# Kernel tuning notes

Measured on AMD Instinct MI355X. Metric: run time of the kernel, lower is better.

The kernel has to match this reference:

```python
import jax, jax.numpy as jnp
import numpy as np

B, T, TA = 16, 512, 1024
D_REG, D_AUD, HID, HEADS = 512, 512, 256, 4
NREG = 4  # mouth, left_eye, right_eye, nose (dict order)
N = NREG * B * T + B * TA  # total graph nodes


def _build_edges():
    # Faithful, vectorized version of build_graph's edge construction (phoneme_times=None).
    bs = np.arange(B)[:, None]
    ts = np.arange(T)[None, :]
    src, dst = [], []
    # cross-region same-timestep edges, all ordered pairs i != j (edge_attr 0)
    for i in range(NREG):
        for j in range(NREG):
            if i != j:
                n1 = i * B * T + bs * T + ts
                n2 = j * B * T + bs * T + ts
                src.append(n1.ravel()); dst.append(n2.ravel())
    # temporal edges within each region (edge_attr 1)
    tt = np.arange(T - 1)[None, :]
    for i in range(NREG):
        n1 = i * B * T + bs * T + tt
        src.append(n1.ravel()); dst.append((n1 + 1).ravel())
    # eye (region idx 1,2) -> audio alignment edges (edge_attr 3)
    t_aud = (np.arange(T)[None, :] * TA) // T
    audio_start = NREG * B * T
    for i in (1, 2):
        n_eye = i * B * T + bs * T + ts
        n_aud = audio_start + bs * TA + t_aud
        src.append(n_eye.ravel()); dst.append(np.broadcast_to(n_aud, (B, T)).ravel())
    # self loops (PyG GATConv default add_self_loops=True)
    loops = np.arange(N)
    src.append(loops); dst.append(loops)
    return np.concatenate(src).astype(np.int32), np.concatenate(dst).astype(np.int32)


def setup_inputs() -> dict:
    key = jax.random.key(0)
    ks = iter(jax.random.split(key, 48))
    def rn(shape, scale=1.0):
        return jax.random.normal(next(ks), shape, dtype=jnp.float32) * jnp.float32(scale)
    src_np, dst_np = _build_edges()
    inp = {
        'mouth': rn((B, T, D_REG)), 'left_eye': rn((B, T, D_REG)),
        'right_eye': rn((B, T, D_REG)), 'nose': rn((B, T, D_REG)),
        'audio_embeddings': rn((B, TA, D_AUD)),
    }
    s = 1.0 / np.sqrt(D_REG)
    for name in ['mouth', 'left_eye', 'right_eye', 'nose']:
        inp['w_' + name] = rn((D_REG, HID), s)
        inp['b_' + name] = jnp.zeros((HID,), jnp.float32)
    inp['w_audio'] = rn((D_AUD, HID), 1.0 / np.sqrt(D_AUD))
    inp['b_audio'] = jnp.zeros((HID,), jnp.float32)
    # GAT layers: layer 0 in=HID, layers 1,2 in=HID*HEADS; layers 0,1 concat, layer 2 averages heads
    dims_in = [HID, HID * HEADS, HID * HEADS]
    for l, din in enumerate(dims_in):
        concat = l < 2
        inp[f'W{l}'] = rn((din, HEADS * HID), 1.0 / np.sqrt(din))
        inp[f'as{l}'] = rn((HEADS, HID), 0.1)
        inp[f'ad{l}'] = rn((HEADS, HID), 0.1)
        inp[f'bias{l}'] = jnp.zeros((HEADS * HID,) if concat else (HID,), jnp.float32)
    inp['ln_g'] = jnp.ones((HID,), jnp.float32)
    inp['ln_b'] = jnp.zeros((HID,), jnp.float32)
    inp['src'] = jnp.asarray(src_np)
    inp['dst'] = jnp.asarray(dst_np)
    return inp


def _gat(x, W, a_s, a_d, bias, src, dst, concat):
    # PyG GATConv (eval mode): gather -> per-head attention softmax over dst -> scatter-add
    H, C = a_s.shape
    h = (x @ W).reshape(-1, H, C)                      # [N,H,C]
    alpha_s = jnp.sum(h * a_s, -1)                     # [N,H]
    alpha_d = jnp.sum(h * a_d, -1)                     # [N,H]
    e = jax.nn.leaky_relu(alpha_s[src] + alpha_d[dst], 0.2)  # [E,H]
    m = jax.ops.segment_max(e, dst, num_segments=N)
    ex = jnp.exp(e - m[dst])
    denom = jax.ops.segment_sum(ex, dst, num_segments=N)
    alpha = ex / (denom[dst] + jnp.float32(1e-16))
    out = jax.ops.segment_sum(h[src] * alpha[:, :, None], dst, num_segments=N)  # [N,H,C]
    out = out.reshape(-1, H * C) if concat else out.mean(1)
    return out + bias


def _forward(mouth, left_eye, right_eye, nose, audio_embeddings,
             w_mouth, b_mouth, w_left_eye, b_left_eye, w_right_eye, b_right_eye,
             w_nose, b_nose, w_audio, b_audio,
             W0, as0, ad0, bias0, W1, as1, ad1, bias1, W2, as2, ad2, bias2,
             ln_g, ln_b, src, dst):
    x = jnp.concatenate([
        (mouth @ w_mouth + b_mouth).reshape(B * T, HID),
        (left_eye @ w_left_eye + b_left_eye).reshape(B * T, HID),
        (right_eye @ w_right_eye + b_right_eye).reshape(B * T, HID),
        (nose @ w_nose + b_nose).reshape(B * T, HID),
        (audio_embeddings @ w_audio + b_audio).reshape(B * TA, HID),
    ], axis=0)                                          # [N,HID]
    x = _gat(x, W0, as0, ad0, bias0, src, dst, True)    # [N,HID*HEADS]
    x = _gat(x, W1, as1, ad1, bias1, src, dst, True)    # [N,HID*HEADS]
    x = _gat(x, W2, as2, ad2, bias2, src, dst, False)   # [N,HID]
    mu = x.mean(-1, keepdims=True)
    var = jnp.mean(jnp.square(x - mu), -1, keepdims=True)
    x = (x - mu) / jnp.sqrt(var + jnp.float32(1e-5)) * ln_g + ln_b
    nodes_pb = NREG * T + TA
    return x.reshape(B, nodes_pb, HID).mean(1)          # [B,HID]


def reference(mouth, left_eye, right_eye, nose, audio_embeddings,
              w_mouth, b_mouth, w_left_eye, b_left_eye, w_right_eye, b_right_eye,
              w_nose, b_nose, w_audio, b_audio,
              W0, as0, ad0, bias0, W1, as1, ad1, bias1, W2, as2, ad2, bias2,
              ln_g, ln_b, src, dst):
    return _forward(mouth, left_eye, right_eye, nose, audio_embeddings,
                    w_mouth, b_mouth, w_left_eye, b_left_eye, w_right_eye, b_right_eye,
                    w_nose, b_nose, w_audio, b_audio,
                    W0, as0, ad0, bias0, W1, as1, ad1, bias1, W2, as2, ad2, bias2,
                    ln_g, ln_b, src, dst)
```

## Files before the change

kernel.cpp:

```cpp
#include <hip/hip_runtime.h>


typedef unsigned short u16;
typedef unsigned int u32;
typedef __bf16 bf16x8 __attribute__((ext_vector_type(8)));
typedef float f32x4 __attribute__((ext_vector_type(4)));

#define ASYNC16(gp, lp)                                                        \
  __builtin_amdgcn_global_load_lds(                                            \
      (const __attribute__((address_space(1))) void*)(gp),                     \
      (__attribute__((address_space(3))) void*)(lp), 16, 0, 0)

__device__ __forceinline__ u16 f2bf(float f) {
  union { float f; u32 u; } v; v.f = f;
  u32 u = v.u + 0x7FFFu + ((v.u >> 16) & 1u);
  return (u16)(u >> 16);
}
__device__ __forceinline__ float bf2f(u16 x) {
  union { u32 u; float f; } v; v.u = ((u32)x) << 16;
  return v.f;
}
__device__ __forceinline__ float4 cvt4(ushort4 s) {
  float4 r; r.x = bf2f(s.x); r.y = bf2f(s.y); r.z = bf2f(s.z); r.w = bf2f(s.w);
  return r;
}
__device__ __forceinline__ float lrelu(float v) { return v > 0.f ? v : 0.2f * v; }
__device__ __forceinline__ float dot4(float4 a, float4 b) {
  return a.x * b.x + a.y * b.y + a.z * b.z + a.w * b.w;
}
__device__ __forceinline__ float wred(float v) {
#pragma unroll
  for (int off = 32; off; off >>= 1) v += __shfl_down(v, off);
  return v;
}
__device__ __forceinline__ float wredx(float v) {
#pragma unroll
  for (int off = 32; off; off >>= 1) v += __shfl_xor(v, off);
  return v;
}

struct PK { const float* W[8]; u16* P[8]; int KB[8]; int NN[8]; int st[9]; };
__global__ __launch_bounds__(256) void pack_kernel(PK p) {
  const int f = blockIdx.x * 4 + (threadIdx.x >> 6);
  const int lane = threadIdx.x & 63;
  int e = 0;
  while (f >= p.st[e + 1]) ++e;
  const int local = f - p.st[e];
  const int KB = p.KB[e], N = p.NN[e];
  const int nt = local / KB, kb = local % KB;
  const float* W = p.W[e] + (size_t)(kb * 32 + (lane >> 4) * 8) * N + nt * 16 + (lane & 15);
  u16* dst = p.P[e] + ((size_t)local * 64 + lane) * 8;
  u16 o[8];
#pragma unroll
  for (int j = 0; j < 8; ++j) o[j] = f2bf(W[(size_t)j * N]);
  *(uint4*)dst = *(uint4*)o;
}

__global__ __launch_bounds__(256) void gemm_kernel(
    const u16* __restrict__ A, const u16* __restrict__ Bp, u16* __restrict__ C,
    int K, int ldc) {
  __shared__ __align__(16) u16 As[2][2][128 * 32];
  const int KB = K >> 5;
  const int KB2 = K >> 6;
  const int w = blockIdx.y * 8 + blockIdx.x;
  const int xcd = w & 7, m = w >> 3;
  const int blockCol = (m & 7) * 128;
  const int blockRow = ((m >> 3) * 8 + xcd) * 128;
  const int tid = threadIdx.x;
  const int wave = tid >> 6, lane = tid & 63;
  const int wr = (wave >> 1) * 64, wc = (wave & 1) * 64;
  const int lr = lane & 15, lq = lane >> 4;
  const int sRow = wave * 16 + (lane >> 2);
  const int sGc = (lane & 3) ^ ((sRow >> 1) & 3);
  const size_t aOff0 = (size_t)(blockRow + sRow) * K + sGc * 8;
  const size_t aOff1 = aOff0 + (size_t)64 * K;
  const int ldsOff0 = wave * 512;
  const int ldsOff1 = 2048 + wave * 512;

  const u16* Bn[4];
#pragma unroll
  for (int ni = 0; ni < 4; ++ni)
    Bn[ni] = Bp + ((size_t)(((blockCol + wc) >> 4) + ni) * KB) * 512 + lane * 8;

  f32x4 acc[4][4] = {};

#pragma unroll
  for (int h = 0; h < 2; ++h) {
    ASYNC16(A + aOff0 + h * 32, As[0][h] + ldsOff0);
    ASYNC16(A + aOff1 + h * 32, As[0][h] + ldsOff1);
  }
  __syncthreads();

  for (int kb2 = 0; kb2 < KB2; ++kb2) {
    const int cb = kb2 & 1;
    bf16x8 bfr[2][4];
#pragma unroll
    for (int h = 0; h < 2; ++h)
#pragma unroll
      for (int ni = 0; ni < 4; ++ni)
        bfr[h][ni] = *(const bf16x8*)(Bn[ni] + (size_t)(kb2 * 2 + h) * 512);
    if (kb2 + 1 < KB2) {
      const size_t k1 = (size_t)(kb2 + 1) * 64;
#pragma unroll
      for (int h = 0; h < 2; ++h) {
        ASYNC16(A + aOff0 + k1 + h * 32, As[cb ^ 1][h] + ldsOff0);
        ASYNC16(A + aOff1 + k1 + h * 32, As[cb ^ 1][h] + ldsOff1);
      }
    }
#pragma unroll
    for (int h = 0; h < 2; ++h) {
      const u16* cur = As[cb][h];
      bf16x8 af[4];
#pragma unroll
      for (int mi = 0; mi < 4; ++mi) {
        const int R = wr + mi * 16 + lr;
        const int cp = lq ^ ((R >> 1) & 3);
        af[mi] = *(const bf16x8*)(cur + R * 32 + cp * 8);
      }
#pragma unroll
      for (int mi = 0; mi < 4; ++mi)
#pragma unroll
        for (int ni = 0; ni < 4; ++ni)
          acc[mi][ni] = __builtin_amdgcn_mfma_f32_16x16x32_bf16(af[mi], bfr[h][ni],
                                                                acc[mi][ni], 0, 0, 0);
    }
    __syncthreads();
  }
#pragma unroll
  for (int mi = 0; mi < 4; ++mi)
#pragma unroll
    for (int ni = 0; ni < 4; ++ni) {
      const int col = blockCol + wc + ni * 16 + lr;
#pragma unroll
      for (int r = 0; r < 4; ++r) {
        const int row = blockRow + wr + mi * 16 + lq * 4 + r;
        C[(size_t)row * ldc + col] = f2bf(acc[mi][ni][r]);
      }
    }
}

struct ProjArgs { const float* x[5]; const u16* w[5]; const float* b[5]; };
__global__ __launch_bounds__(256) void proj_kernel(ProjArgs pa,
                                                   u16* __restrict__ C) {
  __shared__ __align__(16) u16 As[128 * 32];
  const int blockRow = blockIdx.y * 128, blockCol = blockIdx.x * 128;
  const int reg = blockRow >= 32768 ? 4 : (blockRow >> 13);
  const int regBase = reg == 4 ? 32768 : reg * 8192;
  const float* Af = pa.x[reg] + (size_t)(blockRow - regBase) * 512;
  const u16* Bp = pa.w[reg];
  const int tid = threadIdx.x;
  const int wave = tid >> 6, lane = tid & 63;
  const int wr = (wave >> 1) * 64, wc = (wave & 1) * 64;
  const int lr = lane & 15, lq = lane >> 4;
  const int rr = tid >> 2;
  const int cphys = tid & 3;
  const int sGc = cphys ^ ((tid >> 3) & 3);

  const u16* Bn[4];
#pragma unroll
  for (int ni = 0; ni < 4; ++ni)
    Bn[ni] = Bp + ((size_t)(((blockCol + wc) >> 4) + ni) * 16) * 512 + lane * 8;

  f32x4 acc[4][4] = {};

  for (int k0 = 0; k0 < 512; k0 += 32) {
    __syncthreads();
    bf16x8 bfr[4];
#pragma unroll
    for (int ni = 0; ni < 4; ++ni)
      bfr[ni] = *(const bf16x8*)(Bn[ni] + (size_t)k0 * 16);
#pragma unroll
    for (int i = 0; i < 2; ++i) {
      const int row = i * 64 + rr;
      const float* ap = Af + (size_t)row * 512 + k0 + sGc * 8;
      float4 f0 = *(const float4*)(ap);
      float4 f1 = *(const float4*)(ap + 4);
      uint4 pk;
      pk.x = (u32)f2bf(f0.x) | ((u32)f2bf(f0.y) << 16);
      pk.y = (u32)f2bf(f0.z) | ((u32)f2bf(f0.w) << 16);
      pk.z = (u32)f2bf(f1.x) | ((u32)f2bf(f1.y) << 16);
      pk.w = (u32)f2bf(f1.z) | ((u32)f2bf(f1.w) << 16);
      *(uint4*)(&As[row * 32 + cphys * 8]) = pk;
    }
    __syncthreads();
    bf16x8 af[4];
#pragma unroll
    for (int mi = 0; mi < 4; ++mi) {
      const int R = wr + mi * 16 + lr;
      const int cp = lq ^ ((R >> 1) & 3);
      af[mi] = *(const bf16x8*)(&As[R * 32 + cp * 8]);
    }
#pragma unroll
    for (int mi = 0; mi < 4; ++mi)
#pragma unroll
      for (int ni = 0; ni < 4; ++ni)
        acc[mi][ni] = __builtin_amdgcn_mfma_f32_16x16x32_bf16(af[mi], bfr[ni],
                                                              acc[mi][ni], 0, 0, 0);
  }
  const float* bias = pa.b[reg];
#pragma unroll
  for (int mi = 0; mi < 4; ++mi)
#pragma unroll
    for (int ni = 0; ni < 4; ++ni) {
      const int col = blockCol + wc + ni * 16 + lr;
      const float bv = bias[col];
#pragma unroll
      for (int r = 0; r < 4; ++r) {
        const int row = blockRow + wr + mi * 16 + lq * 4 + r;
        C[(size_t)row * 256 + col] = f2bf(acc[mi][ni][r] + bv);
      }
    }
}

template <bool MEAN>
__global__ __launch_bounds__(256) void agg_kernel(
    const u16* __restrict__ h, const float* __restrict__ a_s,
    const float* __restrict__ a_d, const float* __restrict__ bias,
    void* __restrict__ out) {
  extern __shared__ float red[];
  const int tid = threadIdx.x;
  const int head = tid >> 6, lane = tid & 63;
  const int c4 = tid * 4;
  const float4 sa = *(const float4*)(a_s + c4);
  const float4 da = *(const float4*)(a_d + c4);
  __shared__ float asL[4][4], adL[4][4], apL[4][4], aeS[4], aeD[4];
  __shared__ float alpha[4][4][5], alphaA[4][3];

  const int bt = blockIdx.x;
  const int b = bt >> 9, t = bt & 511;
  const bool hasPrev = t > 0;
  const int btp = hasPrev ? bt - 1 : bt;
  const int nodeE = 32768 + b * 1024 + 2 * t;
  const int nodeO = nodeE + 1;

  ushort4 rv[4], rp[4], raeR, raoR;
#pragma unroll
  for (int r = 0; r < 4; ++r)
    rv[r] = *(const ushort4*)(h + (size_t)(r * 8192 + bt) * 1024 + c4);
  raeR = *(const ushort4*)(h + (size_t)nodeE * 1024 + c4);
  raoR = *(const ushort4*)(h + (size_t)nodeO * 1024 + c4);
#pragma unroll
  for (int r = 0; r < 4; ++r)
    rp[r] = *(const ushort4*)(h + (size_t)(r * 8192 + btp) * 1024 + c4);

  float4 hv[4], hp[4];
#pragma unroll
  for (int r = 0; r < 4; ++r) hv[r] = cvt4(rv[r]);
  float4 hae = cvt4(raeR), hao = cvt4(raoR);
#pragma unroll
  for (int r = 0; r < 4; ++r) hp[r] = cvt4(rp[r]);

#pragma unroll
  for (int r = 0; r < 4; ++r) {
    float ss = wred(dot4(hv[r], sa));
    float dd = wred(dot4(hv[r], da));
    float sp = hasPrev ? wred(dot4(hp[r], sa)) : 0.f;
    if (lane == 0) { asL[r][head] = ss; adL[r][head] = dd; apL[r][head] = sp; }
  }
  {
    float se = wred(dot4(hae, sa));
    float de = wred(dot4(hae, da));
    if (lane == 0) { aeS[head] = se; aeD[head] = de; }
  }
  __syncthreads();
  if (tid < 16) {
    const int j = tid >> 2, hh = tid & 3;
    const float ad = adL[j][hh];
    float e[5];
#pragma unroll
    for (int r = 0; r < 4; ++r) e[r] = lrelu(asL[r][hh] + ad);
    int cnt = 4;
    if (hasPrev) { e[4] = lrelu(apL[j][hh] + ad); cnt = 5; }
    float mx = e[0];
    for (int k = 1; k < cnt; ++k) mx = fmaxf(mx, e[k]);
    float s = 0.f, ex[5];
    for (int k = 0; k < cnt; ++k) { ex[k] = __expf(e[k] - mx); s += ex[k]; }
    const float inv = 1.f / (s + 1e-16f);
#pragma unroll
    for (int k = 0; k < 5; ++k) alpha[j][hh][k] = (k < cnt) ? ex[k] * inv : 0.f;
  } else if (tid < 20) {
    const int hh = tid - 16;
    const float ad = aeD[hh];
    const float e0 = lrelu(aeS[hh] + ad);
    const float e1 = lrelu(asL[1][hh] + ad);
    const float e2 = lrelu(asL[2][hh] + ad);
    const float mx = fmaxf(e0, fmaxf(e1, e2));
    const float x0 = __expf(e0 - mx), x1 = __expf(e1 - mx), x2 = __expf(e2 - mx);
    const float inv = 1.f / (x0 + x1 + x2 + 1e-16f);
    alphaA[hh][0] = x0 * inv; alphaA[hh][1] = x1 * inv; alphaA[hh][2] = x2 * inv;
  }
  __syncthreads();

  float4 av[6];
#pragma unroll
  for (int j = 0; j < 4; ++j) {
    const float* al = &alpha[j][head][0];
    float4 acc;
    acc.x = al[0] * hv[0].x + al[1] * hv[1].x + al[2] * hv[2].x + al[3] * hv[3].x;
    acc.y = al[0] * hv[0].y + al[1] * hv[1].y + al[2] * hv[2].y + al[3] * hv[3].y;
    acc.z = al[0] * hv[0].z + al[1] * hv[1].z + al[2] * hv[2].z + al[3] * hv[3].z;
    acc.w = al[0] * hv[0].w + al[1] * hv[1].w + al[2] * hv[2].w + al[3] * hv[3].w;
    if (hasPrev) {
      const float a4 = al[4];
      acc.x += a4 * hp[j].x; acc.y += a4 * hp[j].y;
      acc.z += a4 * hp[j].z; acc.w += a4 * hp[j].w;
    }
    av[j] = acc;
  }
  {
    const float a0 = alphaA[head][0], a1 = alphaA[head][1], a2 = alphaA[head][2];
    float4 acc;
    acc.x = a0 * hae.x + a1 * hv[1].x + a2 * hv[2].x;
    acc.y = a0 * hae.y + a1 * hv[1].y + a2 * hv[2].y;
    acc.z = a0 * hae.z + a1 * hv[1].z + a2 * hv[2].z;
    acc.w = a0 * hae.w + a1 * hv[1].w + a2 * hv[2].w;
    av[4] = acc;
    av[5] = hao;
  }

  if constexpr (!MEAN) {
    const float4 bv = *(const float4*)(bias + c4);
    u16* ob = (u16*)out;
    size_t rows[6];
#pragma unroll
    for (int j = 0; j < 4; ++j) rows[j] = (size_t)(j * 8192 + bt);
    rows[4] = (size_t)nodeE; rows[5] = (size_t)nodeO;
#pragma unroll
    for (int k = 0; k < 6; ++k) {
      ushort4 o;
      o.x = f2bf(av[k].x + bv.x); o.y = f2bf(av[k].y + bv.y);
      o.z = f2bf(av[k].z + bv.z); o.w = f2bf(av[k].w + bv.w);
      *(ushort4*)(ob + rows[k] * 1024 + c4) = o;
    }
  } else {
#pragma unroll
    for (int k = 0; k < 6; ++k) *(float4*)(&red[k * 1024 + c4]) = av[k];
    __syncthreads();
    const float bb = bias[tid];
    float* of = (float*)out;
    size_t rows[6];
#pragma unroll
    for (int j = 0; j < 4; ++j) rows[j] = (size_t)(j * 8192 + bt);
    rows[4] = (size_t)nodeE; rows[5] = (size_t)nodeO;
#pragma unroll
    for (int k = 0; k < 6; ++k) {
      const float v = 0.25f * (red[k * 1024 + tid] + red[k * 1024 + tid + 256] +
                               red[k * 1024 + tid + 512] + red[k * 1024 + tid + 768]) + bb;
      of[rows[k] * 256 + tid] = v;
    }
  }
}

__global__ __launch_bounds__(256) void ln_pool_kernel(
    const float* __restrict__ xf, const float* __restrict__ g,
    const float* __restrict__ bb, float* __restrict__ part) {
  const int tid = threadIdx.x;
  const int wave = tid >> 6, lane = tid & 63;
  const int node0 = blockIdx.x * 64 + wave * 16;
  const float4 g4 = *(const float4*)(g + lane * 4);
  const float4 b4 = *(const float4*)(bb + lane * 4);
  float4 acc = {0.f, 0.f, 0.f, 0.f};
  for (int i = 0; i < 16; ++i) {
    const float4 v = *(const float4*)(xf + (size_t)(node0 + i) * 256 + lane * 4);
    const float s = wredx(v.x + v.y + v.z + v.w);
    const float q = wredx(v.x * v.x + v.y * v.y + v.z * v.z + v.w * v.w);
    const float mean = s * (1.f / 256.f);
    const float var = q * (1.f / 256.f) - mean * mean;
    const float rstd = rsqrtf(var + 1e-5f);
    acc.x += (v.x - mean) * rstd * g4.x + b4.x;
    acc.y += (v.y - mean) * rstd * g4.y + b4.y;
    acc.z += (v.z - mean) * rstd * g4.z + b4.z;
    acc.w += (v.w - mean) * rstd * g4.w + b4.w;
  }
  *(float4*)(part + (size_t)(blockIdx.x * 4 + wave) * 256 + lane * 4) = acc;
}

__global__ __launch_bounds__(256) void pool2_kernel(const float* __restrict__ part,
                                                    float* __restrict__ out) {
  const int chunk = blockIdx.x;
  const int c = threadIdx.x;
  float s = 0.f;
  for (int i = 0; i < 192; ++i) s += part[(size_t)(chunk * 192 + i) * 256 + c];
  out[chunk * 256 + c] = s * (1.f / 3072.f);
}

extern "C" void kernel_launch(void* const* d_in, const int* in_sizes, int n_in,
                              void* d_out, int out_size, void* d_ws, size_t ws_size,
                              hipStream_t stream) {
  const float* x_reg[4] = {(const float*)d_in[0], (const float*)d_in[1],
                           (const float*)d_in[2], (const float*)d_in[3]};
  const float* audio = (const float*)d_in[4];
  const float* w_reg[4] = {(const float*)d_in[5], (const float*)d_in[7],
                           (const float*)d_in[9], (const float*)d_in[11]};
  const float* b_reg[4] = {(const float*)d_in[6], (const float*)d_in[8],
                           (const float*)d_in[10], (const float*)d_in[12]};
  const float* w_aud = (const float*)d_in[13];
  const float* b_aud = (const float*)d_in[14];
  const float* Wl[3] = {(const float*)d_in[15], (const float*)d_in[19],
                        (const float*)d_in[23]};
  const float* as_in[3] = {(const float*)d_in[16], (const float*)d_in[20],
                           (const float*)d_in[24]};
  const float* ad_in[3] = {(const float*)d_in[17], (const float*)d_in[21],
                           (const float*)d_in[25]};
  const float* bias_l[3] = {(const float*)d_in[18], (const float*)d_in[22],
                            (const float*)d_in[26]};
  const float* ln_g = (const float*)d_in[27];
  const float* ln_b = (const float*)d_in[28];

  char* ws = (char*)d_ws;
  u16* h_bf = (u16*)ws;
  float* part = (float*)ws;
  u16* xb = (u16*)(ws + 100663296);
  float* xf = (float*)xb;
  u16* wt = (u16*)(ws + 201326592);

  u16* wtp[5];
  for (int r = 0; r < 5; ++r) wtp[r] = wt + (size_t)r * 131072;
  u16* wt0 = wt + 655360;
  u16* wt1 = wt + 917504;
  u16* wt2 = wt + 1966080;

  PK pk;
  for (int r = 0; r < 4; ++r) { pk.W[r] = w_reg[r]; pk.P[r] = wtp[r]; pk.KB[r] = 16; pk.NN[r] = 256; }
  pk.W[4] = w_aud; pk.P[4] = wtp[4]; pk.KB[4] = 16; pk.NN[4] = 256;
  pk.W[5] = Wl[0]; pk.P[5] = wt0; pk.KB[5] = 8;  pk.NN[5] = 1024;
  pk.W[6] = Wl[1]; pk.P[6] = wt1; pk.KB[6] = 32; pk.NN[6] = 1024;
  pk.W[7] = Wl[2]; pk.P[7] = wt2; pk.KB[7] = 32; pk.NN[7] = 1024;
  pk.st[0] = 0;
  {
    const int nfr[8] = {256, 256, 256, 256, 256, 512, 2048, 2048};
    int acc = 0;
    for (int e = 0; e < 8; ++e) { acc += nfr[e]; pk.st[e + 1] = acc; }
  }
  pack_kernel<<<pk.st[8] / 4, 256, 0, stream>>>(pk);

  ProjArgs pa;
  for (int r = 0; r < 4; ++r) { pa.x[r] = x_reg[r]; pa.w[r] = wtp[r]; pa.b[r] = b_reg[r]; }
  pa.x[4] = audio; pa.w[4] = wtp[4]; pa.b[4] = b_aud;
  proj_kernel<<<dim3(2, 384), 256, 0, stream>>>(pa, xb);

  const u16* wl[3] = {wt0, wt1, wt2};
  const int Kl[3] = {256, 1024, 1024};
  const size_t dynLds = 6 * 1024 * sizeof(float);
  for (int l = 0; l < 3; ++l) {
    gemm_kernel<<<dim3(8, 384), 256, 0, stream>>>(xb, wl[l], h_bf, Kl[l], 1024);
    if (l < 2)
      agg_kernel<false><<<8192, 256, 0, stream>>>(h_bf, as_in[l], ad_in[l],
                                                  bias_l[l], xb);
    else
      agg_kernel<true><<<8192, 256, dynLds, stream>>>(h_bf, as_in[l], ad_in[l],
                                                      bias_l[l], xf);
  }

  ln_pool_kernel<<<768, 256, 0, stream>>>(xf, ln_g, ln_b, part);
  pool2_kernel<<<16, 256, 0, stream>>>(part, (float*)d_out);
}
```

Baseline: 613.5 us.

## Process two timesteps per aggregation block, reusing previous-step rows and swizzling block order

Each aggregation block now handles two consecutive timesteps. The first step's region rows serve as the second step's 'previous' rows, so four row loads per pair are not repeated, and launch count halves. Block IDs are permuted so that concurrently running blocks are spread across batches and timesteps, and the second step's rows are prefetched early. The layer-norm pooling kernel also reduces its four waves in shared memory before writing partials, which shrinks the final pool pass. The trade-off is higher register pressure and an extra barrier per block.

```diff
diff --git a/kernel.cpp b/kernel.cpp
--- a/kernel.cpp
+++ b/kernel.cpp
@@ -226,127 +226,146 @@
   __shared__ float asL[4][4], adL[4][4], apL[4][4], aeS[4], aeD[4];
   __shared__ float alpha[4][4][5], alphaA[4][3];
 
-  const int bt = blockIdx.x;
-  const int b = bt >> 9, t = bt & 511;
-  const bool hasPrev = t > 0;
-  const int btp = hasPrev ? bt - 1 : bt;
-  const int nodeE = 32768 + b * 1024 + 2 * t;
-  const int nodeO = nodeE + 1;
-
-  ushort4 rv[4], rp[4], raeR, raoR;
+  const int bid = blockIdx.x;
+  const int pid = ((bid & 7) << 9) | (bid >> 3);
+  const int bt0 = pid * 2;
+  const int b = bt0 >> 9, t0 = bt0 & 511;
+  const bool hasPrev0 = t0 > 0;
+  const int btp = hasPrev0 ? bt0 - 1 : bt0;
+  const int nodeE0 = 32768 + b * 1024 + 2 * t0;
+
+  ushort4 rv0[4], rp[4], rae0, rao0, rv1[4], rae1, rao1;
 #pragma unroll
   for (int r = 0; r < 4; ++r)
-    rv[r] = *(const ushort4*)(h + (size_t)(r * 8192 + bt) * 1024 + c4);
-  raeR = *(const ushort4*)(h + (size_t)nodeE * 1024 + c4);
-  raoR = *(const ushort4*)(h + (size_t)nodeO * 1024 + c4);
+    rv0[r] = *(const ushort4*)(h + (size_t)(r * 8192 + bt0) * 1024 + c4);
+  rae0 = *(const ushort4*)(h + (size_t)nodeE0 * 1024 + c4);
+  rao0 = *(const ushort4*)(h + (size_t)(nodeE0 + 1) * 1024 + c4);
 #pragma unroll
   for (int r = 0; r < 4; ++r)
     rp[r] = *(const ushort4*)(h + (size_t)(r * 8192 + btp) * 1024 + c4);
-
-  float4 hv[4], hp[4];
-#pragma unroll
-  for (int r = 0; r < 4; ++r) hv[r] = cvt4(rv[r]);
-  float4 hae = cvt4(raeR), hao = cvt4(raoR);
+#pragma unroll
+  for (int r = 0; r < 4; ++r)
+    rv1[r] = *(const ushort4*)(h + (size_t)(r * 8192 + bt0 + 1) * 1024 + c4);
+  rae1 = *(const ushort4*)(h + (size_t)(nodeE0 + 2) * 1024 + c4);
+  rao1 = *(const ushort4*)(h + (size_t)(nodeE0 + 3) * 1024 + c4);
+
+  float4 hv[4], hp[4], hae, hao;
+#pragma unroll
+  for (int r = 0; r < 4; ++r) hv[r] = cvt4(rv0[r]);
+  hae = cvt4(rae0); hao = cvt4(rao0);
 #pragma unroll
   for (int r = 0; r < 4; ++r) hp[r] = cvt4(rp[r]);
 
 #pragma unroll
-  for (int r = 0; r < 4; ++r) {
-    float ss = wred(dot4(hv[r], sa));
-    float dd = wred(dot4(hv[r], da));
-    float sp = hasPrev ? wred(dot4(hp[r], sa)) : 0.f;
-    if (lane == 0) { asL[r][head] = ss; adL[r][head] = dd; apL[r][head] = sp; }
-  }
-  {
-    float se = wred(dot4(hae, sa));
-    float de = wred(dot4(hae, da));
-    if (lane == 0) { aeS[head] = se; aeD[head] = de; }
-  }
-  __syncthreads();
-  if (tid < 16) {
-    const int j = tid >> 2, hh = tid & 3;
-    const float ad = adL[j][hh];
-    float e[5];
-#pragma unroll
-    for (int r = 0; r < 4; ++r) e[r] = lrelu(asL[r][hh] + ad);
-    int cnt = 4;
-    if (hasPrev) { e[4] = lrelu(apL[j][hh] + ad); cnt = 5; }
-    float mx = e[0];
-    for (int k = 1; k < cnt; ++k) mx = fmaxf(mx, e[k]);
-    float s = 0.f, ex[5];
-    for (int k = 0; k < cnt; ++k) { ex[k] = __expf(e[k] - mx); s += ex[k]; }
-    const float inv = 1.f / (s + 1e-16f);
-#pragma unroll
-    for (int k = 0; k < 5; ++k) alpha[j][hh][k] = (k < cnt) ? ex[k] * inv : 0.f;
-  } else if (tid < 20) {
-    const int hh = tid - 16;
-    const float ad = aeD[hh];
-    const float e0 = lrelu(aeS[hh] + ad);
-    const float e1 = lrelu(asL[1][hh] + ad);
-    const float e2 = lrelu(asL[2][hh] + ad);
-    const float mx = fmaxf(e0, fmaxf(e1, e2));
-    const float x0 = __expf(e0 - mx), x1 = __expf(e1 - mx), x2 = __expf(e2 - mx);
-    const float inv = 1.f / (x0 + x1 + x2 + 1e-16f);
-    alphaA[hh][0] = x0 * inv; alphaA[hh][1] = x1 * inv; alphaA[hh][2] = x2 * inv;
-  }
-  __syncthreads();
-
-  float4 av[6];
-#pragma unroll
-  for (int j = 0; j < 4; ++j) {
-    const float* al = &alpha[j][head][0];
-    float4 acc;
-    acc.x = al[0] * hv[0].x + al[1] * hv[1].x + al[2] * hv[2].x + al[3] * hv[3].x;
-    acc.y = al[0] * hv[0].y + al[1] * hv[1].y + al[2] * hv[2].y + al[3] * hv[3].y;
-    acc.z = al[0] * hv[0].z + al[1] * hv[1].z + al[2] * hv[2].z + al[3] * hv[3].z;
-    acc.w = al[0] * hv[0].w + al[1] * hv[1].w + al[2] * hv[2].w + al[3] * hv[3].w;
-    if (hasPrev) {
-      const float a4 = al[4];
-      acc.x += a4 * hp[j].x; acc.y += a4 * hp[j].y;
-      acc.z += a4 * hp[j].z; acc.w += a4 * hp[j].w;
-    }
-    av[j] = acc;
-  }
-  {
-    const float a0 = alphaA[head][0], a1 = alphaA[head][1], a2 = alphaA[head][2];
-    float4 acc;
-    acc.x = a0 * hae.x + a1 * hv[1].x + a2 * hv[2].x;
-    acc.y = a0 * hae.y + a1 * hv[1].y + a2 * hv[2].y;
-    acc.z = a0 * hae.z + a1 * hv[1].z + a2 * hv[2].z;
-    acc.w = a0 * hae.w + a1 * hv[1].w + a2 * hv[2].w;
-    av[4] = acc;
-    av[5] = hao;
-  }
-
-  if constexpr (!MEAN) {
-    const float4 bv = *(const float4*)(bias + c4);
-    u16* ob = (u16*)out;
+  for (int slot = 0; slot < 2; ++slot) {
+    const bool hasPrev = (slot == 1) ? true : hasPrev0;
+    const int bt = bt0 + slot;
+    const int nodeE = nodeE0 + 2 * slot;
+
+#pragma unroll
+    for (int r = 0; r < 4; ++r) {
+      float ss = wred(dot4(hv[r], sa));
+      float dd = wred(dot4(hv[r], da));
+      float sp = hasPrev ? wred(dot4(hp[r], sa)) : 0.f;
+      if (lane == 0) { asL[r][head] = ss; adL[r][head] = dd; apL[r][head] = sp; }
+    }
+    {
+      float se = wred(dot4(hae, sa));
+      float de = wred(dot4(hae, da));
+      if (lane == 0) { aeS[head] = se; aeD[head] = de; }
+    }
+    __syncthreads();
+    if (tid < 16) {
+      const int j = tid >> 2, hh = tid & 3;
+      const float ad = adL[j][hh];
+      float e[5];
+#pragma unroll
+      for (int r = 0; r < 4; ++r) e[r] = lrelu(asL[r][hh] + ad);
+      int cnt = 4;
+      if (hasPrev) { e[4] = lrelu(apL[j][hh] + ad); cnt = 5; }
+      float mx = e[0];
+      for (int k = 1; k < cnt; ++k) mx = fmaxf(mx, e[k]);
+      float s = 0.f, ex[5];
+      for (int k = 0; k < cnt; ++k) { ex[k] = __expf(e[k] - mx); s += ex[k]; }
+      const float inv = 1.f / (s + 1e-16f);
+#pragma unroll
+      for (int k = 0; k < 5; ++k) alpha[j][hh][k] = (k < cnt) ? ex[k] * inv : 0.f;
+    } else if (tid < 20) {
+      const int hh = tid - 16;
+      const float ad = aeD[hh];
+      const float e0 = lrelu(aeS[hh] + ad);
+      const float e1 = lrelu(asL[1][hh] + ad);
+      const float e2 = lrelu(asL[2][hh] + ad);
+      const float mx = fmaxf(e0, fmaxf(e1, e2));
+      const float x0 = __expf(e0 - mx), x1 = __expf(e1 - mx), x2 = __expf(e2 - mx);
+      const float inv = 1.f / (x0 + x1 + x2 + 1e-16f);
+      alphaA[hh][0] = x0 * inv; alphaA[hh][1] = x1 * inv; alphaA[hh][2] = x2 * inv;
+    }
+    __syncthreads();
+
+    float4 av[6];
+#pragma unroll
+    for (int j = 0; j < 4; ++j) {
+      const float* al = &alpha[j][head][0];
+      float4 acc;
+      acc.x = al[0] * hv[0].x + al[1] * hv[1].x + al[2] * hv[2].x + al[3] * hv[3].x;
+      acc.y = al[0] * hv[0].y + al[1] * hv[1].y + al[2] * hv[2].y + al[3] * hv[3].y;
+      acc.z = al[0] * hv[0].z + al[1] * hv[1].z + al[2] * hv[2].z + al[3] * hv[3].z;
+      acc.w = al[0] * hv[0].w + al[1] * hv[1].w + al[2] * hv[2].w + al[3] * hv[3].w;
+      if (hasPrev) {
+        const float a4 = al[4];
+        acc.x += a4 * hp[j].x; acc.y += a4 * hp[j].y;
+        acc.z += a4 * hp[j].z; acc.w += a4 * hp[j].w;
+      }
+      av[j] = acc;
+    }
+    {
+      const float a0 = alphaA[head][0], a1 = alphaA[head][1], a2 = alphaA[head][2];
+      float4 acc;
+      acc.x = a0 * hae.x + a1 * hv[1].x + a2 * hv[2].x;
+      acc.y = a0 * hae.y + a1 * hv[1].y + a2 * hv[2].y;
+      acc.z = a0 * hae.z + a1 * hv[1].z + a2 * hv[2].z;
+      acc.w = a0 * hae.w + a1 * hv[1].w + a2 * hv[2].w;
+      av[4] = acc;
+      av[5] = hao;
+    }
+
     size_t rows[6];
 #pragma unroll
     for (int j = 0; j < 4; ++j) rows[j] = (size_t)(j * 8192 + bt);
-    rows[4] = (size_t)nodeE; rows[5] = (size_t)nodeO;
-#pragma unroll
-    for (int k = 0; k < 6; ++k) {
-      ushort4 o;
-      o.x = f2bf(av[k].x + bv.x); o.y = f2bf(av[k].y + bv.y);
-      o.z = f2bf(av[k].z + bv.z); o.w = f2bf(av[k].w + bv.w);
-      *(ushort4*)(ob + rows[k] * 1024 + c4) = o;
-    }
-  } else {
-#pragma unroll
-    for (int k = 0; k < 6; ++k) *(float4*)(&red[k * 1024 + c4]) = av[k];
-    __syncthreads();
-    const float bb = bias[tid];
-    float* of = (float*)out;
-    size_t rows[6];
-#pragma unroll
-    for (int j = 0; j < 4; ++j) rows[j] = (size_t)(j * 8192 + bt);
-    rows[4] = (size_t)nodeE; rows[5] = (size_t)nodeO;
-#pragma unroll
-    for (int k = 0; k < 6; ++k) {
-      const float v = 0.25f * (red[k * 1024 + tid] + red[k * 1024 + tid + 256] +
-                               red[k * 1024 + tid + 512] + red[k * 1024 + tid + 768]) + bb;
-      of[rows[k] * 256 + tid] = v;
+    rows[4] = (size_t)nodeE; rows[5] = (size_t)(nodeE + 1);
+
+    if constexpr (!MEAN) {
+      const float4 bv = *(const float4*)(bias + c4);
+      u16* ob = (u16*)out;
+#pragma unroll
+      for (int k = 0; k < 6; ++k) {
+        ushort4 o;
+        o.x = f2bf(av[k].x + bv.x); o.y = f2bf(av[k].y + bv.y);
+        o.z = f2bf(av[k].z + bv.z); o.w = f2bf(av[k].w + bv.w);
+        *(ushort4*)(ob + rows[k] * 1024 + c4) = o;
+      }
+    } else {
+#pragma unroll
+      for (int k = 0; k < 6; ++k) *(float4*)(&red[k * 1024 + c4]) = av[k];
+      __syncthreads();
+      const float bb = bias[tid];
+      float* of = (float*)out;
+#pragma unroll
+      for (int k = 0; k < 6; ++k) {
+        const float v = 0.25f * (red[k * 1024 + tid] + red[k * 1024 + tid + 256] +
+                                 red[k * 1024 + tid + 512] + red[k * 1024 + tid + 768]) + bb;
+        of[rows[k] * 256 + tid] = v;
+      }
+    }
+
+    if (slot == 0) {
+#pragma unroll
+      for (int r = 0; r < 4; ++r) hp[r] = hv[r];
+#pragma unroll
+      for (int r = 0; r < 4; ++r) hv[r] = cvt4(rv1[r]);
+      hae = cvt4(rae1); hao = cvt4(rao1);
+      __syncthreads();
     }
   }
 }
@@ -354,6 +373,7 @@
 __global__ __launch_bounds__(256) void ln_pool_kernel(
     const float* __restrict__ xf, const float* __restrict__ g,
     const float* __restrict__ bb, float* __restrict__ part) {
+  __shared__ float sh[1024];
   const int tid = threadIdx.x;
   const int wave = tid >> 6, lane = tid & 63;
   const int node0 = blockIdx.x * 64 + wave * 16;
@@ -372,7 +392,10 @@
     acc.z += (v.z - mean) * rstd * g4.z + b4.z;
     acc.w += (v.w - mean) * rstd * g4.w + b4.w;
   }
-  *(float4*)(part + (size_t)(blockIdx.x * 4 + wave) * 256 + lane * 4) = acc;
+  *(float4*)(&sh[wave * 256 + lane * 4]) = acc;
+  __syncthreads();
+  const float s = sh[tid] + sh[256 + tid] + sh[512 + tid] + sh[768 + tid];
+  part[(size_t)blockIdx.x * 256 + tid] = s;
 }
 
 __global__ __launch_bounds__(256) void pool2_kernel(const float* __restrict__ part,
@@ -380,7 +403,7 @@
   const int chunk = blockIdx.x;
   const int c = threadIdx.x;
   float s = 0.f;
-  for (int i = 0; i < 192; ++i) s += part[(size_t)(chunk * 192 + i) * 256 + c];
+  for (int i = 0; i < 48; ++i) s += part[(size_t)(chunk * 48 + i) * 256 + c];
   out[chunk * 256 + c] = s * (1.f / 3072.f);
 }
 
@@ -445,10 +468,10 @@
   for (int l = 0; l < 3; ++l) {
     gemm_kernel<<<dim3(8, 384), 256, 0, stream>>>(xb, wl[l], h_bf, Kl[l], 1024);
     if (l < 2)
-      agg_kernel<false><<<8192, 256, 0, stream>>>(h_bf, as_in[l], ad_in[l],
+      agg_kernel<false><<<4096, 256, 0, stream>>>(h_bf, as_in[l], ad_in[l],
                                                   bias_l[l], xb);
     else
-      agg_kernel<true><<<8192, 256, dynLds, stream>>>(h_bf, as_in[l], ad_in[l],
+      agg_kernel<true><<<4096, 256, dynLds, stream>>>(h_bf, as_in[l], ad_in[l],
                                                       bias_l[l], xf);
   }
 
```

After: 611.6 us. Within noise of the previous version (-0.3%).
